# Kernel optimization log

Hardware: AMD Instinct MI355X
Metric: run time of the kernel (lower is better)

The kernel has to match this reference:

```python
import jax, jax.numpy as jnp
import numpy as np

H, T, E = 8, 2048, 512


def setup_inputs() -> dict:
    key = jax.random.key(0)
    ks = jax.random.split(key, 11)
    s_e = 1.0 / np.sqrt(E)
    s_f = 1.0 / np.sqrt(H * T)
    return {
        "x": jax.random.normal(ks[0], (T, E), jnp.float32),
        "y": jax.random.normal(ks[1], (T, E), jnp.float32),
        "z": jax.random.normal(ks[2], (T, E), jnp.float32),
        "Wq": jax.random.normal(ks[3], (H, E, E), jnp.float32) * s_e,
        "bq": jax.random.normal(ks[4], (H, E), jnp.float32) * s_e,
        "Wk": jax.random.normal(ks[5], (H, E, E), jnp.float32) * s_e,
        "bk": jax.random.normal(ks[6], (H, E), jnp.float32) * s_e,
        "Wv": jax.random.normal(ks[7], (H, E, E), jnp.float32) * s_e,
        "bv": jax.random.normal(ks[8], (H, E), jnp.float32) * s_e,
        "Wf": jax.random.normal(ks[9], (T, H * T), jnp.float32) * s_f,
        "bf": jax.random.normal(ks[10], (T,), jnp.float32) * s_f,
    }


def reference(x, y, z, Wq, bq, Wk, bk, Wv, bv, Wf, bf):
    # Per-head projections: torch Linear is x @ W.T + b, W is [out,in]
    q = jnp.einsum("se,hfe->hsf", x, Wq) + bq[:, None, :]  # [H,T,E]
    k = jnp.einsum("se,hfe->hsf", y, Wk) + bk[:, None, :]
    v = jnp.einsum("se,hfe->hsf", z, Wv) + bv[:, None, :]
    # Scores scaled by sqrt(num query rows) = sqrt(T), as in the source
    scores = jnp.einsum("hsf,htf->hst", q, k) / jnp.sqrt(jnp.asarray(T, x.dtype))
    att = jax.nn.softmax(scores, axis=-1)
    heads_out = jnp.einsum("hst,htf->hsf", att, v)  # [H,T,E]
    concat = heads_out.reshape(H * T, E)  # cat along dim 0
    # finalLinear applied to concat.T: [E, H*T] @ Wf.T -> [E, T], then transpose
    final = (concat.T @ Wf.T + bf).T  # [T, E]
    residual = final + z
    # Manual per-row LayerNorm: (x - mean) / sqrt(std^2 + 1e-4), population std
    mean = jnp.mean(residual, axis=1, keepdims=True)
    var = jnp.var(residual, axis=1, keepdims=True)
    return (residual - mean) / jnp.sqrt(var + 1e-4)
```

## Files before the change

kernel.cpp:

```cpp
#include <hip/hip_runtime.h>
#include <hip/hip_bf16.h>
#include <cstdint>


#define HH 8
#define TT 2048
#define EE 512
#define HT (HH * TT)
#define HE (HH * EE)

typedef __bf16 bf16_t;
typedef __attribute__((ext_vector_type(8))) __bf16 bf16x8;
typedef __attribute__((ext_vector_type(4))) float f32x4;

__device__ __forceinline__ void gld_lds16(const bf16_t* __restrict__ g, bf16_t* l) {
  __builtin_amdgcn_global_load_lds(
      (const __attribute__((address_space(1))) unsigned int*)g,
      (__attribute__((address_space(3))) unsigned int*)l, 16, 0, 0);
}

__device__ __forceinline__ bf16x8 cvt8(float4 u, float4 v) {
  bf16x8 o;
  o[0] = (__bf16)u.x; o[1] = (__bf16)u.y; o[2] = (__bf16)u.z; o[3] = (__bf16)u.w;
  o[4] = (__bf16)v.x; o[5] = (__bf16)v.y; o[6] = (__bf16)v.z; o[7] = (__bf16)v.w;
  return o;
}

template <typename AT, typename CT>
__global__ __launch_bounds__(256) void mfma_gemm_nt(
    const AT* __restrict__ A, const bf16_t* __restrict__ B, CT* __restrict__ C,
    const float* __restrict__ bias_m, const float* __restrict__ bias_n,
    int K, int lda, int ldb, int ldc,
    int64_t sA, int64_t sB, int64_t sC, int64_t sBM, int64_t sBN) {
  const int gx = gridDim.x, gy = gridDim.y;
  const int nwg = gx * gy * (int)gridDim.z;
  const int lin = blockIdx.x + gx * (blockIdx.y + gy * blockIdx.z);
  const int qn = nwg >> 3, rn = nwg & 7;
  const int xcd = lin & 7, sub = lin >> 3;
  const int wgid = (xcd < rn ? xcd * (qn + 1) : rn * (qn + 1) + (xcd - rn) * qn) + sub;
  const int bx = wgid % gx;
  const int t1 = wgid / gx;
  const int by = t1 % gy;
  const int z = t1 / gy;

  A += z * sA;
  B += z * sB;
  C += z * sC;
  if (bias_m) bias_m += z * sBM;
  if (bias_n) bias_n += z * sBN;

  const int m0 = bx * 128;
  const int n0 = by * 128;
  const int tid = threadIdx.x;

  __shared__ bf16_t sAb[2][128 * 32];
  __shared__ bf16_t sBb[2][128 * 32];

  const int srow = tid >> 2;
  const int scol = (tid & 3) * 8;
  const AT* a0 = A + (int64_t)(m0 + srow) * lda + scol;
  const AT* a1 = a0 + (int64_t)64 * lda;
  const bf16_t* b0 = B + (int64_t)(n0 + srow) * ldb + scol;
  const bf16_t* b1 = b0 + (int64_t)64 * ldb;

  const int wave = tid >> 6;
  const int lane = tid & 63;
  const int wm = (wave >> 1) * 64;
  const int wn = (wave & 1) * 64;
  const int fr = lane & 15;
  const int qd = lane >> 4;

  f32x4 acc[4][4];
#pragma unroll
  for (int i = 0; i < 4; i++)
#pragma unroll
    for (int j = 0; j < 4; j++) acc[i][j] = (f32x4){0.f, 0.f, 0.f, 0.f};

  float4 pa[4];

#define STAGE_B(buf, kt)                              \
  do {                                                \
    gld_lds16(b0 + (kt), &sBb[buf][tid * 8]);         \
    gld_lds16(b1 + (kt), &sBb[buf][2048 + tid * 8]);  \
  } while (0)

#define STAGE_A_BF16(buf, kt)                         \
  do {                                                \
    gld_lds16(a0 + (kt), &sAb[buf][tid * 8]);         \
    gld_lds16(a1 + (kt), &sAb[buf][2048 + tid * 8]);  \
  } while (0)

#define LOAD_A_F32(kt)                                \
  do {                                                \
    pa[0] = ((const float4*)(a0 + (kt)))[0];          \
    pa[1] = ((const float4*)(a0 + (kt)))[1];          \
    pa[2] = ((const float4*)(a1 + (kt)))[0];          \
    pa[3] = ((const float4*)(a1 + (kt)))[1];          \
  } while (0)

#define WRITE_A_F32(buf)                                      \
  do {                                                        \
    *(bf16x8*)&sAb[buf][tid * 8] = cvt8(pa[0], pa[1]);        \
    *(bf16x8*)&sAb[buf][2048 + tid * 8] = cvt8(pa[2], pa[3]); \
  } while (0)

#define COMPUTE(buf)                                                                   \
  do {                                                                                 \
    bf16x8 af[4], bf_[4];                                                              \
    _Pragma("unroll") for (int i = 0; i < 4; i++)                                      \
        af[i] = *(const bf16x8*)&sAb[buf][(wm + i * 16 + fr) * 32 + qd * 8];           \
    _Pragma("unroll") for (int j = 0; j < 4; j++)                                      \
        bf_[j] = *(const bf16x8*)&sBb[buf][(wn + j * 16 + fr) * 32 + qd * 8];          \
    _Pragma("unroll") for (int i = 0; i < 4; i++)                                      \
        _Pragma("unroll") for (int j = 0; j < 4; j++)                                  \
            acc[i][j] =                                                                \
                __builtin_amdgcn_mfma_f32_16x16x32_bf16(af[i], bf_[j], acc[i][j], 0, 0, 0); \
  } while (0)

  if constexpr (sizeof(AT) == 2) {
    STAGE_A_BF16(0, 0);
  } else {
    LOAD_A_F32(0);
    WRITE_A_F32(0);
  }
  STAGE_B(0, 0);
  __syncthreads();

  for (int kt = 0; kt < K; kt += 64) {
    if constexpr (sizeof(AT) == 2) {
      STAGE_A_BF16(1, kt + 32);
    } else {
      LOAD_A_F32(kt + 32);
    }
    STAGE_B(1, kt + 32);
    COMPUTE(0);
    if constexpr (sizeof(AT) == 4) WRITE_A_F32(1);
    __syncthreads();

    const bool more = (kt + 64) < K;
    if (more) {
      if constexpr (sizeof(AT) == 2) {
        STAGE_A_BF16(0, kt + 64);
      } else {
        LOAD_A_F32(kt + 64);
      }
      STAGE_B(0, kt + 64);
    }
    COMPUTE(1);
    if constexpr (sizeof(AT) == 4) {
      if (more) WRITE_A_F32(0);
    }
    __syncthreads();
  }

#undef STAGE_B
#undef STAGE_A_BF16
#undef LOAD_A_F32
#undef WRITE_A_F32
#undef COMPUTE

#pragma unroll
  for (int i = 0; i < 4; i++) {
    const int row0 = m0 + wm + i * 16 + qd * 4;
#pragma unroll
    for (int j = 0; j < 4; j++) {
      const int col = n0 + wn + j * 16 + fr;
      const float bn = bias_n ? bias_n[col] : 0.f;
#pragma unroll
      for (int r = 0; r < 4; r++) {
        const float bm = bias_m ? bias_m[row0 + r] : 0.f;
        C[(int64_t)(row0 + r) * ldc + col] = (CT)(acc[i][j][r] + bn + bm);
      }
    }
  }
}

__global__ __launch_bounds__(256) void cvt_bf16(const float* __restrict__ s,
                                                bf16_t* __restrict__ d) {
  const int64_t i = ((int64_t)blockIdx.x * 256 + threadIdx.x) * 8;
  float4 u = ((const float4*)(s + i))[0];
  float4 v = ((const float4*)(s + i))[1];
  *(bf16x8*)(d + i) = cvt8(u, v);
}

__global__ __launch_bounds__(256) void softmax_rows(bf16_t* __restrict__ S) {
  const float scale = 0.022097086912079608f;
  bf16_t* p = S + (int64_t)blockIdx.x * TT;
  const int tid = threadIdx.x;
  bf16x8 in = *(const bf16x8*)(p + tid * 8);
  float v[8];
  float mx = -1e30f;
#pragma unroll
  for (int i = 0; i < 8; i++) {
    v[i] = (float)in[i] * scale;
    mx = fmaxf(mx, v[i]);
  }
#pragma unroll
  for (int o = 32; o > 0; o >>= 1) mx = fmaxf(mx, __shfl_xor(mx, o));
  __shared__ float redm[4], reds[4];
  if ((tid & 63) == 0) redm[tid >> 6] = mx;
  __syncthreads();
  mx = fmaxf(fmaxf(redm[0], redm[1]), fmaxf(redm[2], redm[3]));
  float sum = 0.f;
#pragma unroll
  for (int i = 0; i < 8; i++) {
    v[i] = __expf(v[i] - mx);
    sum += v[i];
  }
#pragma unroll
  for (int o = 32; o > 0; o >>= 1) sum += __shfl_xor(sum, o);
  if ((tid & 63) == 0) reds[tid >> 6] = sum;
  __syncthreads();
  sum = reds[0] + reds[1] + reds[2] + reds[3];
  const float inv = 1.0f / sum;
  bf16x8 o8;
#pragma unroll
  for (int i = 0; i < 8; i++) o8[i] = (__bf16)(v[i] * inv);
  *(bf16x8*)(p + tid * 8) = o8;
}

__global__ __launch_bounds__(256) void ln_res(const float* __restrict__ F,
                                              const float* __restrict__ Z,
                                              const float* __restrict__ BF,
                                              float* __restrict__ O, int np) {
  const int row = blockIdx.x;
  const int tid = threadIdx.x;
  const int64_t off = (int64_t)row * EE + tid;
  float a = 0.f, b = 0.f;
  for (int pz = 0; pz < np; pz++) {
    const float* f = F + (int64_t)pz * TT * EE;
    a += f[off];
    b += f[off + 256];
  }
  const float bft = BF[row];
  a += bft + Z[off];
  b += bft + Z[off + 256];
  float s = a + b, ss = a * a + b * b;
#pragma unroll
  for (int w = 32; w > 0; w >>= 1) {
    s += __shfl_xor(s, w);
    ss += __shfl_xor(ss, w);
  }
  __shared__ float rs[4], rss[4];
  if ((tid & 63) == 0) {
    rs[tid >> 6] = s;
    rss[tid >> 6] = ss;
  }
  __syncthreads();
  s = rs[0] + rs[1] + rs[2] + rs[3];
  ss = rss[0] + rss[1] + rss[2] + rss[3];
  const float mean = s * (1.0f / EE);
  const float var = ss * (1.0f / EE) - mean * mean;
  const float inv = rsqrtf(var + 1e-4f);
  float* o = O + (int64_t)row * EE;
  o[tid] = (a - mean) * inv;
  o[tid + 256] = (b - mean) * inv;
}

extern "C" void kernel_launch(void* const* d_in, const int* in_sizes, int n_in,
                              void* d_out, int out_size, void* d_ws, size_t ws_size,
                              hipStream_t stream) {
  const float* x = (const float*)d_in[0];
  const float* y = (const float*)d_in[1];
  const float* z = (const float*)d_in[2];
  const float* Wq = (const float*)d_in[3];
  const float* bq = (const float*)d_in[4];
  const float* Wk = (const float*)d_in[5];
  const float* bk = (const float*)d_in[6];
  const float* Wv = (const float*)d_in[7];
  const float* bv = (const float*)d_in[8];
  const float* Wf = (const float*)d_in[9];
  const float* bfb = (const float*)d_in[10];
  float* out = (float*)d_out;

  const size_t MB = 1ull << 20;
  char* p = (char*)d_ws;

  const int64_t nTE = (int64_t)TT * EE;
  const int64_t nW = (int64_t)HH * EE * EE;

  if (ws_size >= 151 * MB) {
    bf16_t* xb = (bf16_t*)(p + 0 * MB);
    bf16_t* yb = (bf16_t*)(p + 2 * MB);
    bf16_t* zb = (bf16_t*)(p + 4 * MB);
    bf16_t* Wqb = (bf16_t*)(p + 6 * MB);
    bf16_t* Wkb = (bf16_t*)(p + 10 * MB);
    bf16_t* Wvb = (bf16_t*)(p + 14 * MB);
    bf16_t* q = (bf16_t*)(p + 18 * MB);
    bf16_t* k = (bf16_t*)(p + 34 * MB);
    bf16_t* vT = (bf16_t*)(p + 50 * MB);
    bf16_t* att = (bf16_t*)(p + 66 * MB);
    bf16_t* hoT = (bf16_t*)(p + 130 * MB);
    float* finp = (float*)(p + 66 * MB);

    cvt_bf16<<<nTE / 2048, 256, 0, stream>>>(x, xb);
    cvt_bf16<<<nTE / 2048, 256, 0, stream>>>(y, yb);
    cvt_bf16<<<nTE / 2048, 256, 0, stream>>>(z, zb);
    cvt_bf16<<<nW / 2048, 256, 0, stream>>>(Wq, Wqb);
    cvt_bf16<<<nW / 2048, 256, 0, stream>>>(Wk, Wkb);
    cvt_bf16<<<nW / 2048, 256, 0, stream>>>(Wv, Wvb);

    mfma_gemm_nt<bf16_t, bf16_t><<<dim3(16, 32, 1), 256, 0, stream>>>(
        xb, Wqb, q, nullptr, bq, EE, EE, EE, HE, 0, 0, 0, 0, 0);
    mfma_gemm_nt<bf16_t, bf16_t><<<dim3(16, 32, 1), 256, 0, stream>>>(
        yb, Wkb, k, nullptr, bk, EE, EE, EE, HE, 0, 0, 0, 0, 0);
    mfma_gemm_nt<bf16_t, bf16_t><<<dim3(32, 16, 1), 256, 0, stream>>>(
        Wvb, zb, vT, bv, nullptr, EE, EE, EE, TT, 0, 0, 0, 0, 0);
    mfma_gemm_nt<bf16_t, bf16_t><<<dim3(16, 16, 8), 256, 0, stream>>>(
        q, k, att, nullptr, nullptr, EE, HE, HE, TT, EE, EE, (int64_t)TT * TT, 0, 0);
    softmax_rows<<<HH * TT, 256, 0, stream>>>(att);
    mfma_gemm_nt<bf16_t, bf16_t><<<dim3(4, 16, 8), 256, 0, stream>>>(
        vT, att, hoT, nullptr, nullptr, TT, TT, TT, HT, (int64_t)EE * TT, (int64_t)TT * TT,
        (int64_t)TT, 0, 0);
    mfma_gemm_nt<float, float><<<dim3(16, 4, 16), 256, 0, stream>>>(
        Wf, hoT, finp, nullptr, nullptr, HT / 16, HT, HT, EE, HT / 16, HT / 16,
        (int64_t)TT * EE, 0, 0);
    ln_res<<<TT, 256, 0, stream>>>(finp, z, bfb, out, 16);
  } else {
    bf16_t* xb = (bf16_t*)(p + 0 * MB);
    bf16_t* yb = (bf16_t*)(p + 2 * MB);
    bf16_t* zb = (bf16_t*)(p + 4 * MB);
    bf16_t* Wqb = (bf16_t*)(p + 6 * MB);
    bf16_t* Wkb = (bf16_t*)(p + 10 * MB);
    bf16_t* Wvb = (bf16_t*)(p + 14 * MB);
    bf16_t* qh = (bf16_t*)(p + 18 * MB);
    bf16_t* kh = (bf16_t*)(p + 20 * MB);
    bf16_t* vTh = (bf16_t*)(p + 22 * MB);
    bf16_t* att = (bf16_t*)(p + 24 * MB);
    bf16_t* hoT = (bf16_t*)(p + 32 * MB);
    float* finp = (float*)(p + 0 * MB);

    cvt_bf16<<<nTE / 2048, 256, 0, stream>>>(x, xb);
    cvt_bf16<<<nTE / 2048, 256, 0, stream>>>(y, yb);
    cvt_bf16<<<nTE / 2048, 256, 0, stream>>>(z, zb);
    cvt_bf16<<<nW / 2048, 256, 0, stream>>>(Wq, Wqb);
    cvt_bf16<<<nW / 2048, 256, 0, stream>>>(Wk, Wkb);
    cvt_bf16<<<nW / 2048, 256, 0, stream>>>(Wv, Wvb);

    for (int h = 0; h < HH; h++) {
      const bf16_t* Wq_h = Wqb + (int64_t)h * EE * EE;
      const bf16_t* Wk_h = Wkb + (int64_t)h * EE * EE;
      const bf16_t* Wv_h = Wvb + (int64_t)h * EE * EE;
      mfma_gemm_nt<bf16_t, bf16_t><<<dim3(16, 4, 1), 256, 0, stream>>>(
          xb, Wq_h, qh, nullptr, bq + h * EE, EE, EE, EE, EE, 0, 0, 0, 0, 0);
      mfma_gemm_nt<bf16_t, bf16_t><<<dim3(16, 4, 1), 256, 0, stream>>>(
          yb, Wk_h, kh, nullptr, bk + h * EE, EE, EE, EE, EE, 0, 0, 0, 0, 0);
      mfma_gemm_nt<bf16_t, bf16_t><<<dim3(4, 16, 1), 256, 0, stream>>>(
          Wv_h, zb, vTh, bv + h * EE, nullptr, EE, EE, EE, TT, 0, 0, 0, 0, 0);
      mfma_gemm_nt<bf16_t, bf16_t><<<dim3(16, 16, 1), 256, 0, stream>>>(
          qh, kh, att, nullptr, nullptr, EE, EE, EE, TT, 0, 0, 0, 0, 0);
      softmax_rows<<<TT, 256, 0, stream>>>(att);
      mfma_gemm_nt<bf16_t, bf16_t><<<dim3(4, 16, 1), 256, 0, stream>>>(
          vTh, att, hoT + (int64_t)h * TT, nullptr, nullptr, TT, TT, TT, HT, 0, 0, 0, 0, 0);
    }
    mfma_gemm_nt<float, float><<<dim3(16, 4, 8), 256, 0, stream>>>(
        Wf, hoT, finp, nullptr, nullptr, HT / 8, HT, HT, EE, HT / 8, HT / 8,
        (int64_t)TT * EE, 0, 0);
    ln_res<<<TT, 256, 0, stream>>>(finp, z, bfb, out, 8);
  }
}
```

Baseline: 509.0 us.

## Widen GEMM to 512 threads with 64-deep K tiles and XOR-swizzled LDS

```diff
diff --git a/kernel.cpp b/kernel.cpp
--- a/kernel.cpp
+++ b/kernel.cpp
@@ -27,7 +27,7 @@
 }
 
 template <typename AT, typename CT>
-__global__ __launch_bounds__(256) void mfma_gemm_nt(
+__global__ __launch_bounds__(512, 4) void mfma_gemm_nt(
     const AT* __restrict__ A, const bf16_t* __restrict__ B, CT* __restrict__ C,
     const float* __restrict__ bias_m, const float* __restrict__ bias_n,
     int K, int lda, int ldb, int ldc,
@@ -53,68 +53,78 @@
   const int n0 = by * 128;
   const int tid = threadIdx.x;
 
-  __shared__ bf16_t sAb[2][128 * 32];
-  __shared__ bf16_t sBb[2][128 * 32];
-
-  const int srow = tid >> 2;
-  const int scol = (tid & 3) * 8;
-  const AT* a0 = A + (int64_t)(m0 + srow) * lda + scol;
+  __shared__ bf16_t sAb[2][128 * 64];
+  __shared__ bf16_t sBb[2][128 * 64];
+
+  const int srow = tid >> 3;
+  const int sc = tid & 7;
+  const int csw = (sc ^ (srow & 7)) * 8;
+  const AT* a0 = A + (int64_t)(m0 + srow) * lda + csw;
   const AT* a1 = a0 + (int64_t)64 * lda;
-  const bf16_t* b0 = B + (int64_t)(n0 + srow) * ldb + scol;
+  const bf16_t* b0 = B + (int64_t)(n0 + srow) * ldb + csw;
   const bf16_t* b1 = b0 + (int64_t)64 * ldb;
 
   const int wave = tid >> 6;
   const int lane = tid & 63;
-  const int wm = (wave >> 1) * 64;
-  const int wn = (wave & 1) * 64;
+  const int wm = (wave >> 2) * 64;
+  const int wn = (wave & 3) * 32;
   const int fr = lane & 15;
   const int qd = lane >> 4;
-
-  f32x4 acc[4][4];
+  const int cx0 = ((0 * 4 + qd) ^ (fr & 7)) * 8;
+  const int cx1 = ((1 * 4 + qd) ^ (fr & 7)) * 8;
+
+  f32x4 acc[4][2];
 #pragma unroll
   for (int i = 0; i < 4; i++)
 #pragma unroll
-    for (int j = 0; j < 4; j++) acc[i][j] = (f32x4){0.f, 0.f, 0.f, 0.f};
+    for (int j = 0; j < 2; j++) acc[i][j] = (f32x4){0.f, 0.f, 0.f, 0.f};
 
   float4 pa[4];
 
-#define STAGE_B(buf, kt)                              \
-  do {                                                \
-    gld_lds16(b0 + (kt), &sBb[buf][tid * 8]);         \
-    gld_lds16(b1 + (kt), &sBb[buf][2048 + tid * 8]);  \
-  } while (0)
-
-#define STAGE_A_BF16(buf, kt)                         \
-  do {                                                \
-    gld_lds16(a0 + (kt), &sAb[buf][tid * 8]);         \
-    gld_lds16(a1 + (kt), &sAb[buf][2048 + tid * 8]);  \
-  } while (0)
-
-#define LOAD_A_F32(kt)                                \
-  do {                                                \
-    pa[0] = ((const float4*)(a0 + (kt)))[0];          \
-    pa[1] = ((const float4*)(a0 + (kt)))[1];          \
-    pa[2] = ((const float4*)(a1 + (kt)))[0];          \
-    pa[3] = ((const float4*)(a1 + (kt)))[1];          \
+#define STAGE_B(buf, kt)                                   \
+  do {                                                     \
+    gld_lds16(b0 + (kt), &sBb[buf][tid * 8]);              \
+    gld_lds16(b1 + (kt), &sBb[buf][4096 + tid * 8]);       \
+  } while (0)
+
+#define STAGE_A_BF16(buf, kt)                              \
+  do {                                                     \
+    gld_lds16(a0 + (kt), &sAb[buf][tid * 8]);              \
+    gld_lds16(a1 + (kt), &sAb[buf][4096 + tid * 8]);       \
+  } while (0)
+
+#define LOAD_A_F32(kt)                                     \
+  do {                                                     \
+    pa[0] = ((const float4*)(a0 + (kt)))[0];               \
+    pa[1] = ((const float4*)(a0 + (kt)))[1];               \
+    pa[2] = ((const float4*)(a1 + (kt)))[0];               \
+    pa[3] = ((const float4*)(a1 + (kt)))[1];               \
   } while (0)
 
 #define WRITE_A_F32(buf)                                      \
   do {                                                        \
     *(bf16x8*)&sAb[buf][tid * 8] = cvt8(pa[0], pa[1]);        \
-    *(bf16x8*)&sAb[buf][2048 + tid * 8] = cvt8(pa[2], pa[3]); \
-  } while (0)
-
-#define COMPUTE(buf)                                                                   \
-  do {                                                                                 \
-    bf16x8 af[4], bf_[4];                                                              \
-    _Pragma("unroll") for (int i = 0; i < 4; i++)                                      \
-        af[i] = *(const bf16x8*)&sAb[buf][(wm + i * 16 + fr) * 32 + qd * 8];           \
-    _Pragma("unroll") for (int j = 0; j < 4; j++)                                      \
-        bf_[j] = *(const bf16x8*)&sBb[buf][(wn + j * 16 + fr) * 32 + qd * 8];          \
-    _Pragma("unroll") for (int i = 0; i < 4; i++)                                      \
-        _Pragma("unroll") for (int j = 0; j < 4; j++)                                  \
-            acc[i][j] =                                                                \
-                __builtin_amdgcn_mfma_f32_16x16x32_bf16(af[i], bf_[j], acc[i][j], 0, 0, 0); \
+    *(bf16x8*)&sAb[buf][4096 + tid * 8] = cvt8(pa[2], pa[3]); \
+  } while (0)
+
+#define COMPUTE(buf)                                                                    \
+  do {                                                                                  \
+    bf16x8 af[2][4], bfr[2][2];                                                         \
+    _Pragma("unroll") for (int i = 0; i < 4; i++) {                                     \
+      const int ar = (wm + i * 16 + fr) * 64;                                           \
+      af[0][i] = *(const bf16x8*)&sAb[buf][ar + cx0];                                   \
+      af[1][i] = *(const bf16x8*)&sAb[buf][ar + cx1];                                   \
+    }                                                                                   \
+    _Pragma("unroll") for (int j = 0; j < 2; j++) {                                     \
+      const int br = (wn + j * 16 + fr) * 64;                                           \
+      bfr[0][j] = *(const bf16x8*)&sBb[buf][br + cx0];                                  \
+      bfr[1][j] = *(const bf16x8*)&sBb[buf][br + cx1];                                  \
+    }                                                                                   \
+    _Pragma("unroll") for (int ks = 0; ks < 2; ks++)                                    \
+        _Pragma("unroll") for (int i = 0; i < 4; i++)                                   \
+            _Pragma("unroll") for (int j = 0; j < 2; j++)                               \
+                acc[i][j] = __builtin_amdgcn_mfma_f32_16x16x32_bf16(                    \
+                    af[ks][i], bfr[ks][j], acc[i][j], 0, 0, 0);                         \
   } while (0)
 
   if constexpr (sizeof(AT) == 2) {
@@ -126,25 +136,25 @@
   STAGE_B(0, 0);
   __syncthreads();
 
-  for (int kt = 0; kt < K; kt += 64) {
+  for (int kt = 0; kt < K; kt += 128) {
     if constexpr (sizeof(AT) == 2) {
-      STAGE_A_BF16(1, kt + 32);
+      STAGE_A_BF16(1, kt + 64);
     } else {
-      LOAD_A_F32(kt + 32);
-    }
-    STAGE_B(1, kt + 32);
+      LOAD_A_F32(kt + 64);
+    }
+    STAGE_B(1, kt + 64);
     COMPUTE(0);
     if constexpr (sizeof(AT) == 4) WRITE_A_F32(1);
     __syncthreads();
 
-    const bool more = (kt + 64) < K;
+    const bool more = (kt + 128) < K;
     if (more) {
       if constexpr (sizeof(AT) == 2) {
-        STAGE_A_BF16(0, kt + 64);
+        STAGE_A_BF16(0, kt + 128);
       } else {
-        LOAD_A_F32(kt + 64);
+        LOAD_A_F32(kt + 128);
       }
-      STAGE_B(0, kt + 64);
+      STAGE_B(0, kt + 128);
     }
     COMPUTE(1);
     if constexpr (sizeof(AT) == 4) {
@@ -163,7 +173,7 @@
   for (int i = 0; i < 4; i++) {
     const int row0 = m0 + wm + i * 16 + qd * 4;
 #pragma unroll
-    for (int j = 0; j < 4; j++) {
+    for (int j = 0; j < 2; j++) {
       const int col = n0 + wn + j * 16 + fr;
       const float bn = bias_n ? bias_n[col] : 0.f;
 #pragma unroll
@@ -300,22 +310,22 @@
     cvt_bf16<<<nW / 2048, 256, 0, stream>>>(Wk, Wkb);
     cvt_bf16<<<nW / 2048, 256, 0, stream>>>(Wv, Wvb);
 
-    mfma_gemm_nt<bf16_t, bf16_t><<<dim3(16, 32, 1), 256, 0, stream>>>(
+    mfma_gemm_nt<bf16_t, bf16_t><<<dim3(16, 32, 1), 512, 0, stream>>>(
         xb, Wqb, q, nullptr, bq, EE, EE, EE, HE, 0, 0, 0, 0, 0);
-    mfma_gemm_nt<bf16_t, bf16_t><<<dim3(16, 32, 1), 256, 0, stream>>>(
+    mfma_gemm_nt<bf16_t, bf16_t><<<dim3(16, 32, 1), 512, 0, stream>>>(
         yb, Wkb, k, nullptr, bk, EE, EE, EE, HE, 0, 0, 0, 0, 0);
-    mfma_gemm_nt<bf16_t, bf16_t><<<dim3(32, 16, 1), 256, 0, stream>>>(
+    mfma_gemm_nt<bf16_t, bf16_t><<<dim3(32, 16, 1), 512, 0, stream>>>(
         Wvb, zb, vT, bv, nullptr, EE, EE, EE, TT, 0, 0, 0, 0, 0);
-    mfma_gemm_nt<bf16_t, bf16_t><<<dim3(16, 16, 8), 256, 0, stream>>>(
+    mfma_gemm_nt<bf16_t, bf16_t><<<dim3(16, 16, 8), 512, 0, stream>>>(
         q, k, att, nullptr, nullptr, EE, HE, HE, TT, EE, EE, (int64_t)TT * TT, 0, 0);
     softmax_rows<<<HH * TT, 256, 0, stream>>>(att);
-    mfma_gemm_nt<bf16_t, bf16_t><<<dim3(4, 16, 8), 256, 0, stream>>>(
+    mfma_gemm_nt<bf16_t, bf16_t><<<dim3(4, 16, 8), 512, 0, stream>>>(
         vT, att, hoT, nullptr, nullptr, TT, TT, TT, HT, (int64_t)EE * TT, (int64_t)TT * TT,
         (int64_t)TT, 0, 0);
-    mfma_gemm_nt<float, float><<<dim3(16, 4, 16), 256, 0, stream>>>(
-        Wf, hoT, finp, nullptr, nullptr, HT / 16, HT, HT, EE, HT / 16, HT / 16,
+    mfma_gemm_nt<float, float><<<dim3(16, 4, 8), 512, 0, stream>>>(
+        Wf, hoT, finp, nullptr, nullptr, HT / 8, HT, HT, EE, HT / 8, HT / 8,
         (int64_t)TT * EE, 0, 0);
-    ln_res<<<TT, 256, 0, stream>>>(finp, z, bfb, out, 16);
+    ln_res<<<TT, 256, 0, stream>>>(finp, z, bfb, out, 8);
   } else {
     bf16_t* xb = (bf16_t*)(p + 0 * MB);
     bf16_t* yb = (bf16_t*)(p + 2 * MB);
@@ -341,19 +351,19 @@
       const bf16_t* Wq_h = Wqb + (int64_t)h * EE * EE;
       const bf16_t* Wk_h = Wkb + (int64_t)h * EE * EE;
       const bf16_t* Wv_h = Wvb + (int64_t)h * EE * EE;
-      mfma_gemm_nt<bf16_t, bf16_t><<<dim3(16, 4, 1), 256, 0, stream>>>(
+      mfma_gemm_nt<bf16_t, bf16_t><<<dim3(16, 4, 1), 512, 0, stream>>>(
           xb, Wq_h, qh, nullptr, bq + h * EE, EE, EE, EE, EE, 0, 0, 0, 0, 0);
-      mfma_gemm_nt<bf16_t, bf16_t><<<dim3(16, 4, 1), 256, 0, stream>>>(
+      mfma_gemm_nt<bf16_t, bf16_t><<<dim3(16, 4, 1), 512, 0, stream>>>(
           yb, Wk_h, kh, nullptr, bk + h * EE, EE, EE, EE, EE, 0, 0, 0, 0, 0);
-      mfma_gemm_nt<bf16_t, bf16_t><<<dim3(4, 16, 1), 256, 0, stream>>>(
+      mfma_gemm_nt<bf16_t, bf16_t><<<dim3(4, 16, 1), 512, 0, stream>>>(
           Wv_h, zb, vTh, bv + h * EE, nullptr, EE, EE, EE, TT, 0, 0, 0, 0, 0);
-      mfma_gemm_nt<bf16_t, bf16_t><<<dim3(16, 16, 1), 256, 0, stream>>>(
+      mfma_gemm_nt<bf16_t, bf16_t><<<dim3(16, 16, 1), 512, 0, stream>>>(
           qh, kh, att, nullptr, nullptr, EE, EE, EE, TT, 0, 0, 0, 0, 0);
       softmax_rows<<<TT, 256, 0, stream>>>(att);
-      mfma_gemm_nt<bf16_t, bf16_t><<<dim3(4, 16, 1), 256, 0, stream>>>(
+      mfma_gemm_nt<bf16_t, bf16_t><<<dim3(4, 16, 1), 512, 0, stream>>>(
           vTh, att, hoT + (int64_t)h * TT, nullptr, nullptr, TT, TT, TT, HT, 0, 0, 0, 0, 0);
     }
-    mfma_gemm_nt<float, float><<<dim3(16, 4, 8), 256, 0, stream>>>(
+    mfma_gemm_nt<float, float><<<dim3(16, 4, 8), 512, 0, stream>>>(
         Wf, hoT, finp, nullptr, nullptr, HT / 8, HT, HT, EE, HT / 8, HT / 8,
         (int64_t)TT * EE, 0, 0);
     ln_res<<<TT, 256, 0, stream>>>(finp, z, bfb, out, 8);
```

Result: faster. 430.5 us (-15.4%).
